# Performance work log

Hardware: AMD Instinct MI355X
Metric: run time of the kernel (lower is better)

Reference implementation:

```python
import jax, jax.numpy as jnp
import numpy as np

RADIUS = 0.45


def _square_distance(src, dst):
    # [B,N,C] x [B,M,C] -> [B,N,M] squared Euclidean distances
    d = -2.0 * jnp.einsum('bnc,bmc->bnm', src, dst)
    d = d + jnp.sum(src * src, -1)[:, :, None]
    d = d + jnp.sum(dst * dst, -1)[:, None, :]
    return d


def _query_ball(radius, nsample, xyz):
    # faithful to torch query_ball_point: mark out-of-radius as N, sort, take nsample, fill with first
    B, N, _ = xyz.shape
    sqr = _square_distance(xyz, xyz)  # [B,N,N]
    idx = jnp.where(sqr > radius * radius, N,
                    jnp.arange(N, dtype=jnp.int32)[None, None, :])
    idx = jnp.sort(idx, axis=-1)[:, :, :nsample]  # [B,N,nsample]
    first = idx[:, :, :1]
    return jnp.where(idx == N, first, idx)


def _gather(points, idx):
    # points [B,N,C], idx [B,S,K] -> [B,S,K,C]
    B = points.shape[0]
    return points[jnp.arange(B)[:, None, None], idx]


def _mlp2(g, W1, b1, W2, b2):
    # g: [B,S,K,Cin]; 1x1 conv2d == per-point matmul; relu each layer
    h = jax.nn.relu(jnp.einsum('bskc,oc->bsko', g, W1) + b1)
    h = jax.nn.relu(jnp.einsum('bski,oi->bsko', h, W2) + b2)
    return jnp.max(h, axis=2)  # max over neighbors K -> [B,S,Cout]


def setup_inputs() -> dict:
    key = jax.random.key(0)
    ks = jax.random.split(key, 13)
    B, N = 8, 2048
    s = 0.1
    return {
        'x': jax.random.uniform(ks[0], (B, N, 3), dtype=jnp.float32),
        'W1a': jax.random.normal(ks[1], (32, 3), dtype=jnp.float32) * s,
        'b1a': jnp.zeros((32,), jnp.float32),
        'W2a': jax.random.normal(ks[2], (64, 32), dtype=jnp.float32) * s,
        'b2a': jnp.zeros((64,), jnp.float32),
        'W1b': jax.random.normal(ks[3], (64, 3), dtype=jnp.float32) * s,
        'b1b': jnp.zeros((64,), jnp.float32),
        'W2b': jax.random.normal(ks[4], (128, 64), dtype=jnp.float32) * s,
        'b2b': jnp.zeros((128,), jnp.float32),
        'Wc1': jax.random.normal(ks[5], (64, 3), dtype=jnp.float32) * s,
        'bc1': jnp.zeros((64,), jnp.float32),
        'Wc2': jax.random.normal(ks[6], (256, 128), dtype=jnp.float32) * s,
        'bc2': jnp.zeros((256,), jnp.float32),
    }


def reference(x, W1a, b1a, W2a, b2a, W1b, b1b, W2b, b2b, Wc1, bc1, Wc2, bc2):
    # branch 1: ball query (nsample=64) -> gather -> 1x1 MLP (3->32->64) -> max-pool
    idx1 = _query_ball(RADIUS, 64, x)
    g1 = _mlp2(_gather(x, idx1), W1a, b1a, W2a, b2a)  # [B,N,64]
    g1 = jnp.transpose(g1, (0, 2, 1))                 # [B,64,N]

    # point-wise conv1d 3->64 on raw coords
    xf = jax.nn.relu(jnp.einsum('bnc,oc->bon', x, Wc1) + bc1[None, :, None])
    xf = jnp.concatenate([xf, g1], axis=1)            # [B,128,N]
    xf = jax.nn.relu(jnp.einsum('bcn,oc->bon', xf, Wc2) + bc2[None, :, None])  # [B,256,N]

    # branch 2: ball query (nsample=128) -> gather -> 1x1 MLP (3->64->128) -> max-pool
    idx2 = _query_ball(RADIUS, 128, x)
    g2 = _mlp2(_gather(x, idx2), W1b, b1b, W2b, b2b)  # [B,N,128]
    g2 = jnp.transpose(g2, (0, 2, 1))                 # [B,128,N]

    return jnp.concatenate([xf, g2], axis=1)          # [B,384,N]
```

## Files before the change

kernel.cpp:

```cpp
#include <hip/hip_runtime.h>
#include <cstdint>

#define NPTS 2048
#define NB 8
#define R2C 0.2025f

__device__ __forceinline__ float fmul(float a, float b) { return __fmul_rn(a, b); }
__device__ __forceinline__ float fadd(float a, float b) { return __fadd_rn(a, b); }

__global__ __launch_bounds__(1024) void k_features(
    const float* __restrict__ X,
    const float* __restrict__ W1a, const float* __restrict__ b1a,
    const float* __restrict__ W2a, const float* __restrict__ b2a,
    const float* __restrict__ W1b, const float* __restrict__ b1b,
    const float* __restrict__ W2b, const float* __restrict__ b2b,
    const float* __restrict__ Wc1, const float* __restrict__ bc1,
    float* __restrict__ fa, float* __restrict__ fb, float* __restrict__ v)
{
    __shared__ float fat[64][65];
    __shared__ float fbt[64][129];
    int tid = threadIdx.x;
    int q = __builtin_amdgcn_readfirstlane(tid >> 6);
    int lane = tid & 63;
    int pbase = blockIdx.x * 64;
    int p = pbase + lane;
    int b = p >> 11, i = p & 2047;

    float x0 = X[p * 3 + 0], x1 = X[p * 3 + 1], x2 = X[p * 3 + 2];

    float h[64];
#pragma unroll
    for (int o = 0; o < 32; ++o)
        h[o] = fmaxf(0.f, x0 * W1a[o * 3] + x1 * W1a[o * 3 + 1] + x2 * W1a[o * 3 + 2] + b1a[o]);
#pragma unroll
    for (int oo = 0; oo < 4; ++oo) {
        int o = q * 4 + oo;
        float acc = b2a[o];
#pragma unroll
        for (int k = 0; k < 32; ++k) acc = fmaf(h[k], W2a[o * 32 + k], acc);
        fat[lane][o] = fmaxf(0.f, acc);
    }
#pragma unroll
    for (int o = 0; o < 64; ++o)
        h[o] = fmaxf(0.f, x0 * W1b[o * 3] + x1 * W1b[o * 3 + 1] + x2 * W1b[o * 3 + 2] + b1b[o]);
#pragma unroll
    for (int oo = 0; oo < 8; ++oo) {
        int o = q * 8 + oo;
        float acc = b2b[o];
#pragma unroll
        for (int k = 0; k < 64; ++k) acc = fmaf(h[k], W2b[o * 64 + k], acc);
        fbt[lane][o] = fmaxf(0.f, acc);
    }
    float* vb = v + (size_t)b * 128 * NPTS + i;
#pragma unroll
    for (int oo = 0; oo < 4; ++oo) {
        int o = q * 4 + oo;
        vb[(size_t)o * NPTS] =
            fmaxf(0.f, x0 * Wc1[o * 3] + x1 * Wc1[o * 3 + 1] + x2 * Wc1[o * 3 + 2] + bc1[o]);
    }
    __syncthreads();

#pragma unroll
    for (int r = 0; r < 4; ++r) {
        int idx = r * 1024 + tid;
        int pt = idx >> 6, ch = idx & 63;
        fa[((size_t)(pbase + pt)) * 64 + ch] = fat[pt][ch];
    }
#pragma unroll
    for (int r = 0; r < 8; ++r) {
        int idx = r * 1024 + tid;
        int pt = idx >> 7, ch = idx & 127;
        fb[((size_t)(pbase + pt)) * 128 + ch] = fbt[pt][ch];
    }
}

__global__ __launch_bounds__(1024) void k_neighbors(
    const float* __restrict__ X, const float* __restrict__ fa,
    const float* __restrict__ fb, float* __restrict__ v, float* __restrict__ out)
{
    __shared__ float xs[NPTS * 3];
    __shared__ unsigned short nbr[16][128];
    __shared__ float g1t[64][17];
    __shared__ float g2t[128][17];
    int tid = threadIdx.x;
    int wid = tid >> 6, lane = tid & 63;
    int b = blockIdx.x & 7;
    int i0 = (blockIdx.x >> 3) * 16;
    int i = i0 + wid;

    const float4* xsrc = (const float4*)(X + (size_t)b * NPTS * 3);
    float4* xdst = (float4*)xs;
    for (int t = tid; t < (NPTS * 3 / 4); t += 1024) xdst[t] = xsrc[t];
    __syncthreads();

    float n0 = xs[i * 3], n1 = xs[i * 3 + 1], n2 = xs[i * 3 + 2];
    float nn = fadd(fadd(fmul(n0, n0), fmul(n1, n1)), fmul(n2, n2));

    unsigned long long myword = 0;
    for (int w = 0; w < 32; ++w) {
        int m = (w << 6) | lane;
        float y0 = xs[m * 3], y1 = xs[m * 3 + 1], y2 = xs[m * 3 + 2];
        float dot = fadd(fadd(fmul(n0, y0), fmul(n1, y1)), fmul(n2, y2));
        float mm  = fadd(fadd(fmul(y0, y0), fmul(y1, y1)), fmul(y2, y2));
        float d   = fadd(fadd(fmul(-2.0f, dot), nn), mm);
        unsigned long long bm = __ballot(!(d > R2C));
        if (lane == w) myword = bm;
    }

    int cnt = (lane < 32) ? __popcll(myword) : 0;
    int incl = cnt;
#pragma unroll
    for (int d = 1; d < 32; d <<= 1) {
        int t = __shfl_up(incl, d, 64);
        if (lane >= d) incl += t;
    }
    int pre = incl - cnt;
    if (lane < 32 && cnt && pre < 128) {
        unsigned long long word = myword;
        int r = pre;
        while (word && r < 128) {
            int pb = __builtin_ctzll(word);
            word &= word - 1;
            nbr[wid][r++] = (unsigned short)((lane << 6) | pb);
        }
    }
    int total = __shfl(incl, 31, 64);
    int c1 = min(total, 64);
    int c2 = min(total, 128);
    __syncthreads();

    {
        const float* fab = fa + (size_t)b * NPTS * 64 + lane;
        float g1 = -1e30f;
        int j = 0;
        for (; j + 8 <= c1; j += 8) {
            ushort4 qa = *(const ushort4*)&nbr[wid][j];
            ushort4 qb = *(const ushort4*)&nbr[wid][j + 4];
            float a0 = fab[(size_t)qa.x * 64];
            float a1 = fab[(size_t)qa.y * 64];
            float a2 = fab[(size_t)qa.z * 64];
            float a3 = fab[(size_t)qa.w * 64];
            float a4 = fab[(size_t)qb.x * 64];
            float a5 = fab[(size_t)qb.y * 64];
            float a6 = fab[(size_t)qb.z * 64];
            float a7 = fab[(size_t)qb.w * 64];
            g1 = fmaxf(g1, fmaxf(fmaxf(fmaxf(a0, a1), fmaxf(a2, a3)),
                                 fmaxf(fmaxf(a4, a5), fmaxf(a6, a7))));
        }
        for (; j < c1; ++j) g1 = fmaxf(g1, fab[(size_t)nbr[wid][j] * 64]);
        g1t[lane][wid] = g1;
    }
    {
        const float2* fbb = (const float2*)(fb + (size_t)b * NPTS * 128) + lane;
        float2 g2; g2.x = -1e30f; g2.y = -1e30f;
        int j = 0;
        for (; j + 8 <= c2; j += 8) {
            ushort4 qa = *(const ushort4*)&nbr[wid][j];
            ushort4 qb = *(const ushort4*)&nbr[wid][j + 4];
            float2 a0 = fbb[(size_t)qa.x * 64];
            float2 a1 = fbb[(size_t)qa.y * 64];
            float2 a2 = fbb[(size_t)qa.z * 64];
            float2 a3 = fbb[(size_t)qa.w * 64];
            float2 a4 = fbb[(size_t)qb.x * 64];
            float2 a5 = fbb[(size_t)qb.y * 64];
            float2 a6 = fbb[(size_t)qb.z * 64];
            float2 a7 = fbb[(size_t)qb.w * 64];
            g2.x = fmaxf(g2.x, fmaxf(fmaxf(fmaxf(a0.x, a1.x), fmaxf(a2.x, a3.x)),
                                     fmaxf(fmaxf(a4.x, a5.x), fmaxf(a6.x, a7.x))));
            g2.y = fmaxf(g2.y, fmaxf(fmaxf(fmaxf(a0.y, a1.y), fmaxf(a2.y, a3.y)),
                                     fmaxf(fmaxf(a4.y, a5.y), fmaxf(a6.y, a7.y))));
        }
        for (; j < c2; ++j) {
            float2 a = fbb[(size_t)nbr[wid][j] * 64];
            g2.x = fmaxf(g2.x, a.x); g2.y = fmaxf(g2.y, a.y);
        }
        g2t[2 * lane][wid] = g2.x;
        g2t[2 * lane + 1][wid] = g2.y;
    }
    __syncthreads();

    {
        int ch = tid >> 4, pt = tid & 15;
        v[((size_t)b * 128 + 64 + ch) * NPTS + i0 + pt] = g1t[ch][pt];
    }
#pragma unroll
    for (int r = 0; r < 2; ++r) {
        int idx = r * 1024 + tid;
        int ch = idx >> 4, pt = idx & 15;
        out[((size_t)b * 384 + 256 + ch) * NPTS + i0 + pt] = g2t[ch][pt];
    }
}

__global__ __launch_bounds__(256) void k_conv2(
    const float* __restrict__ v, const float* __restrict__ Wc2,
    const float* __restrict__ bc2, float* __restrict__ out)
{
    __shared__ float vs[128 * 32];
    __shared__ float ws[256 * 33];
    int b = blockIdx.x & 7;
    int nt = (blockIdx.x >> 3) << 5;
    int t = threadIdx.x;
    int n_t = t & 3, o_t = t >> 2;

    const float* vb = v + (size_t)b * 128 * NPTS + nt;
#pragma unroll
    for (int r = 0; r < 4; ++r) {
        int j = r * 256 + t; int k = j >> 3, n4 = j & 7;
        *(float4*)&vs[k * 32 + n4 * 4] = *(const float4*)(vb + (size_t)k * NPTS + n4 * 4);
    }

    float acc[4][8];
#pragma unroll
    for (int r = 0; r < 4; ++r) {
        float bb = bc2[o_t * 4 + r];
#pragma unroll
        for (int n = 0; n < 8; ++n) acc[r][n] = bb;
    }

    for (int kc = 0; kc < 128; kc += 32) {
        __syncthreads();
#pragma unroll
        for (int r = 0; r < 8; ++r) {
            int j = r * 256 + t; int o = j >> 3, c = j & 7;
            float4 wv = *(const float4*)(Wc2 + (size_t)o * 128 + kc + c * 4);
            ws[o * 33 + c * 4 + 0] = wv.x;
            ws[o * 33 + c * 4 + 1] = wv.y;
            ws[o * 33 + c * 4 + 2] = wv.z;
            ws[o * 33 + c * 4 + 3] = wv.w;
        }
        __syncthreads();
#pragma unroll 4
        for (int kk = 0; kk < 32; ++kk) {
            float4 va = *(float4*)&vs[(kc + kk) * 32 + n_t * 8];
            float4 vb4 = *(float4*)&vs[(kc + kk) * 32 + n_t * 8 + 4];
            float vv[8] = {va.x, va.y, va.z, va.w, vb4.x, vb4.y, vb4.z, vb4.w};
            float ww[4];
#pragma unroll
            for (int r = 0; r < 4; ++r) ww[r] = ws[(o_t * 4 + r) * 33 + kk];
#pragma unroll
            for (int r = 0; r < 4; ++r)
#pragma unroll
                for (int n = 0; n < 8; ++n)
                    acc[r][n] = fmaf(ww[r], vv[n], acc[r][n]);
        }
    }

    float* ob = out + ((size_t)b * 384 + o_t * 4) * NPTS + nt + n_t * 8;
#pragma unroll
    for (int r = 0; r < 4; ++r) {
        float4 s0, s1;
        s0.x = fmaxf(0.f, acc[r][0]); s0.y = fmaxf(0.f, acc[r][1]);
        s0.z = fmaxf(0.f, acc[r][2]); s0.w = fmaxf(0.f, acc[r][3]);
        s1.x = fmaxf(0.f, acc[r][4]); s1.y = fmaxf(0.f, acc[r][5]);
        s1.z = fmaxf(0.f, acc[r][6]); s1.w = fmaxf(0.f, acc[r][7]);
        *(float4*)(ob + (size_t)r * NPTS) = s0;
        *(float4*)(ob + (size_t)r * NPTS + 4) = s1;
    }
}

extern "C" void kernel_launch(void* const* d_in, const int* in_sizes, int n_in,
                              void* d_out, int out_size, void* d_ws, size_t ws_size,
                              hipStream_t stream) {
    const float* X   = (const float*)d_in[0];
    const float* W1a = (const float*)d_in[1];
    const float* b1a = (const float*)d_in[2];
    const float* W2a = (const float*)d_in[3];
    const float* b2a = (const float*)d_in[4];
    const float* W1b = (const float*)d_in[5];
    const float* b1b = (const float*)d_in[6];
    const float* W2b = (const float*)d_in[7];
    const float* b2b = (const float*)d_in[8];
    const float* Wc1 = (const float*)d_in[9];
    const float* bc1 = (const float*)d_in[10];
    const float* Wc2 = (const float*)d_in[11];
    const float* bc2 = (const float*)d_in[12];
    float* out = (float*)d_out;

    float* fa = (float*)d_ws;
    float* fb = fa + (size_t)NB * NPTS * 64;
    float* v  = fb + (size_t)NB * NPTS * 128;

    k_features<<<NB * NPTS / 64, 1024, 0, stream>>>(X, W1a, b1a, W2a, b2a,
                                                    W1b, b1b, W2b, b2b, Wc1, bc1,
                                                    fa, fb, v);
    k_neighbors<<<NB * NPTS / 16, 1024, 0, stream>>>(X, fa, fb, v, out);
    k_conv2<<<NB * (NPTS / 32), 256, 0, stream>>>(v, Wc2, bc2, out);
}
```

Baseline: 205.8 us.

## Store per-point MLP features as fp16 and max-pool with packed half gathers

Per-point branch features are now written to the workspace as fp16 pairs. The neighbor max-pool gathers whole 16-byte rows, with several neighbors per wavefront, and reduces with packed f16 max plus cross-lane shuffles. This halves gather traffic and widens the loads. The feature kernel moves to 512 threads with two outputs per FMA loop, and the ball query precomputes squared norms into float4 shared memory. Rounding to fp16 adds error to the max-pooled outputs. The packed max starts from zero, which relies on the features being non-negative after ReLU.

```diff
diff --git a/kernel.cpp b/kernel.cpp
--- a/kernel.cpp
+++ b/kernel.cpp
@@ -1,4 +1,5 @@
 #include <hip/hip_runtime.h>
+#include <hip/hip_fp16.h>
 #include <cstdint>
 
 #define NPTS 2048
@@ -8,17 +9,31 @@
 __device__ __forceinline__ float fmul(float a, float b) { return __fmul_rn(a, b); }
 __device__ __forceinline__ float fadd(float a, float b) { return __fadd_rn(a, b); }
 
-__global__ __launch_bounds__(1024) void k_features(
+__device__ __forceinline__ uint hmax2u(uint a, uint b) {
+    uint r;
+    asm volatile("v_pk_max_f16 %0, %1, %2" : "=v"(r) : "v"(a), "v"(b));
+    return r;
+}
+__device__ __forceinline__ float lo_f(uint u) {
+    __half h = __ushort_as_half((unsigned short)(u & 0xffff));
+    return __half2float(h);
+}
+__device__ __forceinline__ float hi_f(uint u) {
+    __half h = __ushort_as_half((unsigned short)(u >> 16));
+    return __half2float(h);
+}
+
+__global__ __launch_bounds__(512, 4) void k_features(
     const float* __restrict__ X,
     const float* __restrict__ W1a, const float* __restrict__ b1a,
     const float* __restrict__ W2a, const float* __restrict__ b2a,
     const float* __restrict__ W1b, const float* __restrict__ b1b,
     const float* __restrict__ W2b, const float* __restrict__ b2b,
     const float* __restrict__ Wc1, const float* __restrict__ bc1,
-    float* __restrict__ fa, float* __restrict__ fb, float* __restrict__ v)
+    __half* __restrict__ fa, __half* __restrict__ fb, float* __restrict__ v)
 {
-    __shared__ float fat[64][65];
-    __shared__ float fbt[64][129];
+    __shared__ float fat[64 * 33];
+    __shared__ float fbt[64 * 67];
     int tid = threadIdx.x;
     int q = __builtin_amdgcn_readfirstlane(tid >> 6);
     int lane = tid & 63;
@@ -33,52 +48,62 @@
     for (int o = 0; o < 32; ++o)
         h[o] = fmaxf(0.f, x0 * W1a[o * 3] + x1 * W1a[o * 3 + 1] + x2 * W1a[o * 3 + 2] + b1a[o]);
 #pragma unroll
-    for (int oo = 0; oo < 4; ++oo) {
-        int o = q * 4 + oo;
-        float acc = b2a[o];
-#pragma unroll
-        for (int k = 0; k < 32; ++k) acc = fmaf(h[k], W2a[o * 32 + k], acc);
-        fat[lane][o] = fmaxf(0.f, acc);
+    for (int oo = 0; oo < 8; oo += 2) {
+        int o = q * 8 + oo;
+        float a0 = b2a[o], a1 = b2a[o + 1];
+#pragma unroll
+        for (int k = 0; k < 32; ++k) {
+            a0 = fmaf(h[k], W2a[o * 32 + k], a0);
+            a1 = fmaf(h[k], W2a[(o + 1) * 32 + k], a1);
+        }
+        __half2 hh = __floats2half2_rn(fmaxf(0.f, a0), fmaxf(0.f, a1));
+        fat[lane * 33 + q * 4 + (oo >> 1)] = *(float*)&hh;
     }
 #pragma unroll
     for (int o = 0; o < 64; ++o)
         h[o] = fmaxf(0.f, x0 * W1b[o * 3] + x1 * W1b[o * 3 + 1] + x2 * W1b[o * 3 + 2] + b1b[o]);
 #pragma unroll
+    for (int oo = 0; oo < 16; oo += 2) {
+        int o = q * 16 + oo;
+        float a0 = b2b[o], a1 = b2b[o + 1];
+#pragma unroll
+        for (int k = 0; k < 64; ++k) {
+            a0 = fmaf(h[k], W2b[o * 64 + k], a0);
+            a1 = fmaf(h[k], W2b[(o + 1) * 64 + k], a1);
+        }
+        __half2 hh = __floats2half2_rn(fmaxf(0.f, a0), fmaxf(0.f, a1));
+        fbt[lane * 67 + q * 8 + (oo >> 1)] = *(float*)&hh;
+    }
+    float* vb = v + (size_t)b * 128 * NPTS + i;
+#pragma unroll
     for (int oo = 0; oo < 8; ++oo) {
         int o = q * 8 + oo;
-        float acc = b2b[o];
-#pragma unroll
-        for (int k = 0; k < 64; ++k) acc = fmaf(h[k], W2b[o * 64 + k], acc);
-        fbt[lane][o] = fmaxf(0.f, acc);
-    }
-    float* vb = v + (size_t)b * 128 * NPTS + i;
-#pragma unroll
-    for (int oo = 0; oo < 4; ++oo) {
-        int o = q * 4 + oo;
         vb[(size_t)o * NPTS] =
             fmaxf(0.f, x0 * Wc1[o * 3] + x1 * Wc1[o * 3 + 1] + x2 * Wc1[o * 3 + 2] + bc1[o]);
     }
     __syncthreads();
 
+    uint* fau = (uint*)fa;
 #pragma unroll
     for (int r = 0; r < 4; ++r) {
-        int idx = r * 1024 + tid;
-        int pt = idx >> 6, ch = idx & 63;
-        fa[((size_t)(pbase + pt)) * 64 + ch] = fat[pt][ch];
-    }
+        int idx = r * 512 + tid;
+        int pt = idx >> 5, j = idx & 31;
+        fau[((size_t)(pbase + pt)) * 32 + j] = *(uint*)&fat[pt * 33 + j];
+    }
+    uint* fbu = (uint*)fb;
 #pragma unroll
     for (int r = 0; r < 8; ++r) {
-        int idx = r * 1024 + tid;
-        int pt = idx >> 7, ch = idx & 127;
-        fb[((size_t)(pbase + pt)) * 128 + ch] = fbt[pt][ch];
+        int idx = r * 512 + tid;
+        int pt = idx >> 6, j = idx & 63;
+        fbu[((size_t)(pbase + pt)) * 64 + j] = *(uint*)&fbt[pt * 67 + j];
     }
 }
 
 __global__ __launch_bounds__(1024) void k_neighbors(
-    const float* __restrict__ X, const float* __restrict__ fa,
-    const float* __restrict__ fb, float* __restrict__ v, float* __restrict__ out)
+    const float* __restrict__ X, const __half* __restrict__ fa,
+    const __half* __restrict__ fb, float* __restrict__ v, float* __restrict__ out)
 {
-    __shared__ float xs[NPTS * 3];
+    __shared__ float4 xs4[NPTS];
     __shared__ unsigned short nbr[16][128];
     __shared__ float g1t[64][17];
     __shared__ float g2t[128][17];
@@ -88,21 +113,22 @@
     int i0 = (blockIdx.x >> 3) * 16;
     int i = i0 + wid;
 
-    const float4* xsrc = (const float4*)(X + (size_t)b * NPTS * 3);
-    float4* xdst = (float4*)xs;
-    for (int t = tid; t < (NPTS * 3 / 4); t += 1024) xdst[t] = xsrc[t];
+    const float* Xb = X + (size_t)b * NPTS * 3;
+    for (int t = tid; t < NPTS; t += 1024) {
+        float y0 = Xb[3 * t], y1 = Xb[3 * t + 1], y2 = Xb[3 * t + 2];
+        float mm = fadd(fadd(fmul(y0, y0), fmul(y1, y1)), fmul(y2, y2));
+        xs4[t] = make_float4(y0, y1, y2, mm);
+    }
     __syncthreads();
 
-    float n0 = xs[i * 3], n1 = xs[i * 3 + 1], n2 = xs[i * 3 + 2];
-    float nn = fadd(fadd(fmul(n0, n0), fmul(n1, n1)), fmul(n2, n2));
+    float4 cc = xs4[i];
+    float n0 = cc.x, n1 = cc.y, n2 = cc.z, nn = cc.w;
 
     unsigned long long myword = 0;
     for (int w = 0; w < 32; ++w) {
-        int m = (w << 6) | lane;
-        float y0 = xs[m * 3], y1 = xs[m * 3 + 1], y2 = xs[m * 3 + 2];
-        float dot = fadd(fadd(fmul(n0, y0), fmul(n1, y1)), fmul(n2, y2));
-        float mm  = fadd(fadd(fmul(y0, y0), fmul(y1, y1)), fmul(y2, y2));
-        float d   = fadd(fadd(fmul(-2.0f, dot), nn), mm);
+        float4 y = xs4[(w << 6) | lane];
+        float dot = fadd(fadd(fmul(n0, y.x), fmul(n1, y.y)), fmul(n2, y.z));
+        float d   = fadd(fadd(fmul(-2.0f, dot), nn), y.w);
         unsigned long long bm = __ballot(!(d > R2C));
         if (lane == w) myword = bm;
     }
@@ -130,52 +156,64 @@
     __syncthreads();
 
     {
-        const float* fab = fa + (size_t)b * NPTS * 64 + lane;
-        float g1 = -1e30f;
-        int j = 0;
-        for (; j + 8 <= c1; j += 8) {
-            ushort4 qa = *(const ushort4*)&nbr[wid][j];
-            ushort4 qb = *(const ushort4*)&nbr[wid][j + 4];
-            float a0 = fab[(size_t)qa.x * 64];
-            float a1 = fab[(size_t)qa.y * 64];
-            float a2 = fab[(size_t)qa.z * 64];
-            float a3 = fab[(size_t)qa.w * 64];
-            float a4 = fab[(size_t)qb.x * 64];
-            float a5 = fab[(size_t)qb.y * 64];
-            float a6 = fab[(size_t)qb.z * 64];
-            float a7 = fab[(size_t)qb.w * 64];
-            g1 = fmaxf(g1, fmaxf(fmaxf(fmaxf(a0, a1), fmaxf(a2, a3)),
-                                 fmaxf(fmaxf(a4, a5), fmaxf(a6, a7))));
-        }
-        for (; j < c1; ++j) g1 = fmaxf(g1, fab[(size_t)nbr[wid][j] * 64]);
-        g1t[lane][wid] = g1;
+        const uint4* fab = (const uint4*)(fa + (size_t)b * NPTS * 64);
+        int g = lane >> 3, c8 = lane & 7;
+        uint acc0 = 0, acc1 = 0, acc2 = 0, acc3 = 0;
+        int it1 = (c1 + 7) >> 3;
+        for (int j = 0; j < it1; ++j) {
+            int idx = min(j * 8 + g, c1 - 1);
+            int row = nbr[wid][idx];
+            uint4 rr = fab[row * 8 + c8];
+            acc0 = hmax2u(acc0, rr.x);
+            acc1 = hmax2u(acc1, rr.y);
+            acc2 = hmax2u(acc2, rr.z);
+            acc3 = hmax2u(acc3, rr.w);
+        }
+#pragma unroll
+        for (int s = 8; s < 64; s <<= 1) {
+            acc0 = hmax2u(acc0, (uint)__shfl_xor((int)acc0, s, 64));
+            acc1 = hmax2u(acc1, (uint)__shfl_xor((int)acc1, s, 64));
+            acc2 = hmax2u(acc2, (uint)__shfl_xor((int)acc2, s, 64));
+            acc3 = hmax2u(acc3, (uint)__shfl_xor((int)acc3, s, 64));
+        }
+        if (g == 0) {
+            uint a[4] = {acc0, acc1, acc2, acc3};
+#pragma unroll
+            for (int k = 0; k < 4; ++k) {
+                g1t[8 * c8 + 2 * k][wid]     = lo_f(a[k]);
+                g1t[8 * c8 + 2 * k + 1][wid] = hi_f(a[k]);
+            }
+        }
     }
     {
-        const float2* fbb = (const float2*)(fb + (size_t)b * NPTS * 128) + lane;
-        float2 g2; g2.x = -1e30f; g2.y = -1e30f;
-        int j = 0;
-        for (; j + 8 <= c2; j += 8) {
-            ushort4 qa = *(const ushort4*)&nbr[wid][j];
-            ushort4 qb = *(const ushort4*)&nbr[wid][j + 4];
-            float2 a0 = fbb[(size_t)qa.x * 64];
-            float2 a1 = fbb[(size_t)qa.y * 64];
-            float2 a2 = fbb[(size_t)qa.z * 64];
-            float2 a3 = fbb[(size_t)qa.w * 64];
-            float2 a4 = fbb[(size_t)qb.x * 64];
-            float2 a5 = fbb[(size_t)qb.y * 64];
-            float2 a6 = fbb[(size_t)qb.z * 64];
-            float2 a7 = fbb[(size_t)qb.w * 64];
-            g2.x = fmaxf(g2.x, fmaxf(fmaxf(fmaxf(a0.x, a1.x), fmaxf(a2.x, a3.x)),
-                                     fmaxf(fmaxf(a4.x, a5.x), fmaxf(a6.x, a7.x))));
-            g2.y = fmaxf(g2.y, fmaxf(fmaxf(fmaxf(a0.y, a1.y), fmaxf(a2.y, a3.y)),
-                                     fmaxf(fmaxf(a4.y, a5.y), fmaxf(a6.y, a7.y))));
-        }
-        for (; j < c2; ++j) {
-            float2 a = fbb[(size_t)nbr[wid][j] * 64];
-            g2.x = fmaxf(g2.x, a.x); g2.y = fmaxf(g2.y, a.y);
-        }
-        g2t[2 * lane][wid] = g2.x;
-        g2t[2 * lane + 1][wid] = g2.y;
+        const uint4* fbb = (const uint4*)(fb + (size_t)b * NPTS * 128);
+        int g = lane >> 4, c8 = lane & 15;
+        uint acc0 = 0, acc1 = 0, acc2 = 0, acc3 = 0;
+        int it2 = (c2 + 3) >> 2;
+        for (int j = 0; j < it2; ++j) {
+            int idx = min(j * 4 + g, c2 - 1);
+            int row = nbr[wid][idx];
+            uint4 rr = fbb[row * 16 + c8];
+            acc0 = hmax2u(acc0, rr.x);
+            acc1 = hmax2u(acc1, rr.y);
+            acc2 = hmax2u(acc2, rr.z);
+            acc3 = hmax2u(acc3, rr.w);
+        }
+#pragma unroll
+        for (int s = 16; s < 64; s <<= 1) {
+            acc0 = hmax2u(acc0, (uint)__shfl_xor((int)acc0, s, 64));
+            acc1 = hmax2u(acc1, (uint)__shfl_xor((int)acc1, s, 64));
+            acc2 = hmax2u(acc2, (uint)__shfl_xor((int)acc2, s, 64));
+            acc3 = hmax2u(acc3, (uint)__shfl_xor((int)acc3, s, 64));
+        }
+        if (g == 0) {
+            uint a[4] = {acc0, acc1, acc2, acc3};
+#pragma unroll
+            for (int k = 0; k < 4; ++k) {
+                g2t[8 * c8 + 2 * k][wid]     = lo_f(a[k]);
+                g2t[8 * c8 + 2 * k + 1][wid] = hi_f(a[k]);
+            }
+        }
     }
     __syncthreads();
 
@@ -276,13 +314,13 @@
     const float* bc2 = (const float*)d_in[12];
     float* out = (float*)d_out;
 
-    float* fa = (float*)d_ws;
-    float* fb = fa + (size_t)NB * NPTS * 64;
-    float* v  = fb + (size_t)NB * NPTS * 128;
-
-    k_features<<<NB * NPTS / 64, 1024, 0, stream>>>(X, W1a, b1a, W2a, b2a,
-                                                    W1b, b1b, W2b, b2b, Wc1, bc1,
-                                                    fa, fb, v);
+    __half* fa = (__half*)d_ws;
+    __half* fb = fa + (size_t)NB * NPTS * 64;
+    float*  v  = (float*)(fb + (size_t)NB * NPTS * 128);
+
+    k_features<<<NB * NPTS / 64, 512, 0, stream>>>(X, W1a, b1a, W2a, b2a,
+                                                   W1b, b1b, W2b, b2b, Wc1, bc1,
+                                                   fa, fb, v);
     k_neighbors<<<NB * NPTS / 16, 1024, 0, stream>>>(X, fa, fb, v, out);
     k_conv2<<<NB * (NPTS / 32), 256, 0, stream>>>(v, Wc2, bc2, out);
 }
```

Result: faster. 194.0 us (-5.7%).
